# Kernel optimization log

Hardware: AMD Instinct MI355X
Metric: run time of the kernel (lower is better)

## Reference

```python
import jax, jax.numpy as jnp
import numpy as np

B, S, D, H = 2, 2048, 1024, 16
HD = D // H
LAMBDA_INIT = 0.8
EPS = 1e-5


def setup_inputs() -> dict:
    key = jax.random.key(0)
    ks = jax.random.split(key, 14)
    f32 = jnp.float32
    return {
        "inputs": jax.random.normal(ks[0], (B, S, D), f32),
        "attention_mask": jnp.ones((B, S), f32),
        "Wq": jax.random.normal(ks[1], (D, 2 * D), f32) * 0.02,
        "Wk": jax.random.normal(ks[2], (D, 2 * D), f32) * 0.02,
        "Wv": jax.random.normal(ks[3], (D, D), f32) * 0.02,
        "Wo": jax.random.normal(ks[4], (D, D), f32) * 0.02,
        "lam_q1": jax.random.normal(ks[5], (HD,), f32) * 0.1,
        "lam_q2": jax.random.normal(ks[6], (HD,), f32) * 0.1,
        "lam_k1": jax.random.normal(ks[7], (HD,), f32) * 0.1,
        "lam_k2": jax.random.normal(ks[8], (HD,), f32) * 0.1,
        "gn_weight": jnp.ones((D,), f32),
        "gn_bias": jnp.zeros((D,), f32),
        "memory_gate": jax.random.normal(ks[9], (1, H, 1, HD), f32),
        "mem": jnp.zeros((1, H, HD, HD), f32),
        "z": jnp.ones((1, H, HD, 1), f32),
    }


def reference(inputs, attention_mask, Wq, Wk, Wv, Wo, lam_q1, lam_q2, lam_k1, lam_k2,
              gn_weight, gn_bias, memory_gate, mem, z):
    Bv, Sv, Dv = inputs.shape
    scale = 1.0 / jnp.sqrt(jnp.float32(HD))
    q = (inputs @ Wq).reshape(Bv, Sv, H, 2 * HD).transpose(0, 2, 1, 3)  # B,H,S,2hd
    k = (inputs @ Wk).reshape(Bv, Sv, H, 2 * HD).transpose(0, 2, 1, 3)
    v = (inputs @ Wv).reshape(Bv, Sv, H, HD).transpose(0, 2, 1, 3)      # B,H,S,hd
    Q1, Q2 = q[..., :HD], q[..., HD:]
    K1, K2 = k[..., :HD], k[..., HD:]
    pos = jnp.arange(Sv, dtype=jnp.float32)
    slopes = 2.0 ** (-8.0 * jnp.arange(1, H + 1, dtype=jnp.float32) / H)
    alibi = slopes[None, :, None, None] * (pos[:, None] - pos[None, :])[None, None]  # 1,H,S,S
    causal = jnp.triu(jnp.full((Sv, Sv), -1e9, jnp.float32), k=1)
    pad = (1.0 - attention_mask)[:, None, None, :] * -1e9  # B,1,1,S
    def attn(Q, K):
        s = jnp.einsum('bhqd,bhkd->bhqk', Q, K) * scale - alibi + causal + pad
        return jax.nn.softmax(s, axis=-1)
    w1 = attn(Q1, K1)
    w2 = attn(Q2, K2)
    lam = jnp.exp(jnp.dot(lam_q1, lam_k1)) - jnp.exp(jnp.dot(lam_q2, lam_k2)) + LAMBDA_INIT
    diff_w = w1 - lam * w2  # B,H,S,S
    # linear-attention memory read (mem update is dead code w.r.t. output)
    sigma_q = jax.nn.elu(Q1) + 1.0
    mem_values = (sigma_q @ mem) / (sigma_q @ z)  # B,H,S,hd
    gate = jax.nn.sigmoid(memory_gate)
    out = gate * mem_values + (1.0 - gate) * jnp.einsum('bhqk,bhkd->bhqd', diff_w, v)
    # GroupNorm(num_groups=H) over channels-first layout: per (head) group stats over (hd, S)
    x = out.transpose(0, 1, 3, 2)  # B,H,hd,S
    mu = x.mean(axis=(2, 3), keepdims=True)
    var = ((x - mu) ** 2).mean(axis=(2, 3), keepdims=True)
    xn = (x - mu) / jnp.sqrt(var + EPS)
    xn = xn * gn_weight.reshape(1, H, HD, 1) + gn_bias.reshape(1, H, HD, 1)
    y = xn.transpose(0, 3, 1, 2).reshape(Bv, Sv, H * HD) * (1.0 - LAMBDA_INIT)
    return y @ Wo
```

## Files before the change

kernel.cpp:

```cpp
#include <hip/hip_runtime.h>
#include <stdint.h>

#define B_ 2
#define S_ 2048
#define D_ 1024
#define H_ 16
#define HD_ 64
#define NC_ 5120

typedef unsigned short ushort_t;
typedef __bf16 bf16x8_t __attribute__((ext_vector_type(8)));
typedef unsigned short us8 __attribute__((ext_vector_type(8)));
typedef float f32x4 __attribute__((ext_vector_type(4)));

using gq_t = const unsigned int __attribute__((address_space(1)));
using lq_t = unsigned int __attribute__((address_space(3)));

__device__ __forceinline__ unsigned short f2bf(float f) {
    unsigned u = __builtin_bit_cast(unsigned, f);
    u += 0x7fffu + ((u >> 16) & 1u);
    return (unsigned short)(u >> 16);
}
__device__ __forceinline__ float bf2f(unsigned short h) {
    unsigned u = ((unsigned)h) << 16;
    return __builtin_bit_cast(float, u);
}
__device__ __forceinline__ f32x4 mfma16(us8 a, us8 b, f32x4 c) {
    return __builtin_amdgcn_mfma_f32_16x16x32_bf16(
        __builtin_bit_cast(bf16x8_t, a), __builtin_bit_cast(bf16x8_t, b), c, 0, 0, 0);
}
__device__ __forceinline__ void gload16(const void* g, void* l) {
    __builtin_amdgcn_global_load_lds((gq_t*)g, (lq_t*)l, 16, 0, 0);
}

__global__ __launch_bounds__(256) void k_convert_x(const float* __restrict__ X,
                                                   ushort_t* __restrict__ Xb) {
    int i = (blockIdx.x * 256 + threadIdx.x) * 4;
    float4 v = *reinterpret_cast<const float4*>(X + i);
    ushort4 o;
    o.x = f2bf(v.x); o.y = f2bf(v.y); o.z = f2bf(v.z); o.w = f2bf(v.w);
    *reinterpret_cast<ushort4*>(Xb + i) = o;
}

__global__ __launch_bounds__(256) void k_transpose_w(const float* __restrict__ W,
                                                     ushort_t* __restrict__ Bt,
                                                     int N, int n_base) {
    __shared__ float lds[64 * 65];
    int n0 = blockIdx.x * 64, k0 = blockIdx.y * 64;
    int t = threadIdx.x;
#pragma unroll
    for (int i = 0; i < 16; i++) {
        int idx = i * 256 + t;
        int r = idx >> 6, c = idx & 63;
        lds[c * 65 + r] = W[(size_t)(k0 + r) * N + (n0 + c)];
    }
    __syncthreads();
#pragma unroll
    for (int i = 0; i < 16; i++) {
        int idx = i * 256 + t;
        int nn = idx >> 6, k = idx & 63;
        Bt[(size_t)(n_base + n0 + nn) * 1024 + (k0 + k)] = f2bf(lds[nn * 65 + k]);
    }
}

__device__ __forceinline__ void gemm_tile(const ushort_t* __restrict__ A,
                                          const ushort_t* __restrict__ Bt,
                                          int m0, int n0,
                                          ushort_t* ldsA, ushort_t* ldsB,
                                          f32x4 acc[4][4]) {
    const int K = 1024;
    int t = threadIdx.x;
    int w = t >> 6, l = t & 63;
    int wr = (w >> 1) * 64, wc = (w & 1) * 64;
    int lo16 = l & 15, lg = l >> 4;
#pragma unroll
    for (int m = 0; m < 4; m++)
#pragma unroll
        for (int n = 0; n < 4; n++) acc[m][n] = f32x4{0.f, 0.f, 0.f, 0.f};

    for (int k0 = 0; k0 < K; k0 += 64) {
#pragma unroll
        for (int i = 0; i < 4; i++) {
            int c = i * 256 + t;
            int row = c >> 3, co = (c & 7) * 8;
            gload16(A + (size_t)(m0 + row) * K + k0 + co, ldsA + (size_t)c * 8);
            gload16(Bt + (size_t)(n0 + row) * K + k0 + co, ldsB + (size_t)c * 8);
        }
        __syncthreads();
#pragma unroll
        for (int kk = 0; kk < 2; kk++) {
            us8 af[4], bfr[4];
#pragma unroll
            for (int m = 0; m < 4; m++)
                af[m] = *(const us8*)(ldsA + (wr + m * 16 + lo16) * 64 + kk * 32 + lg * 8);
#pragma unroll
            for (int n = 0; n < 4; n++)
                bfr[n] = *(const us8*)(ldsB + (wc + n * 16 + lo16) * 64 + kk * 32 + lg * 8);
#pragma unroll
            for (int m = 0; m < 4; m++)
#pragma unroll
                for (int n = 0; n < 4; n++)
                    acc[m][n] = mfma16(af[m], bfr[n], acc[m][n]);
        }
        __syncthreads();
    }
}

__global__ __launch_bounds__(256) void k_gemm_qkv(const ushort_t* __restrict__ Xb,
                                                  const ushort_t* __restrict__ Wt,
                                                  ushort_t* __restrict__ C) {
    __shared__ __align__(16) ushort_t ldsA[128 * 64];
    __shared__ __align__(16) ushort_t ldsB[128 * 64];
    f32x4 acc[4][4];
    int m0 = blockIdx.y * 128, n0 = blockIdx.x * 128;
    gemm_tile(Xb, Wt, m0, n0, ldsA, ldsB, acc);
    int t = threadIdx.x, w = t >> 6, l = t & 63;
    int wr = (w >> 1) * 64, wc = (w & 1) * 64, lo16 = l & 15, lg = l >> 4;
#pragma unroll
    for (int m = 0; m < 4; m++)
#pragma unroll
        for (int n = 0; n < 4; n++)
#pragma unroll
            for (int r = 0; r < 4; r++)
                C[(size_t)(m0 + wr + m * 16 + lg * 4 + r) * NC_ + (n0 + wc + n * 16 + lo16)] =
                    f2bf(acc[m][n][r]);
}

__global__ __launch_bounds__(256) void k_gemm_out(const ushort_t* __restrict__ Yb,
                                                  const ushort_t* __restrict__ Wot,
                                                  float* __restrict__ Out) {
    __shared__ __align__(16) ushort_t ldsA[128 * 64];
    __shared__ __align__(16) ushort_t ldsB[128 * 64];
    f32x4 acc[4][4];
    int m0 = blockIdx.y * 128, n0 = blockIdx.x * 128;
    gemm_tile(Yb, Wot, m0, n0, ldsA, ldsB, acc);
    int t = threadIdx.x, w = t >> 6, l = t & 63;
    int wr = (w >> 1) * 64, wc = (w & 1) * 64, lo16 = l & 15, lg = l >> 4;
#pragma unroll
    for (int m = 0; m < 4; m++)
#pragma unroll
        for (int n = 0; n < 4; n++)
#pragma unroll
            for (int r = 0; r < 4; r++)
                Out[(size_t)(m0 + wr + m * 16 + lg * 4 + r) * 1024 + (n0 + wc + n * 16 + lo16)] =
                    acc[m][n][r];
}

__global__ __launch_bounds__(256) void k_transpose_v(const ushort_t* __restrict__ C,
                                                     ushort_t* __restrict__ Vt) {
    __shared__ ushort_t lds[64 * 72];
    int bh = blockIdx.x, s0 = blockIdx.y * 64;
    int b = bh >> 4, h = bh & 15;
    const ushort_t* src = C + (size_t)(b * S_ + s0) * NC_ + 4096 + h * 64;
    ushort_t* dst = Vt + (size_t)bh * HD_ * S_ + s0;
    int t = threadIdx.x;
#pragma unroll
    for (int i = 0; i < 16; i++) {
        int idx = i * 256 + t;
        int s = idx >> 6, d = idx & 63;
        lds[d * 72 + s] = src[(size_t)s * NC_ + d];
    }
    __syncthreads();
#pragma unroll
    for (int i = 0; i < 16; i++) {
        int idx = i * 256 + t;
        int d = idx >> 6, s = idx & 63;
        dst[(size_t)d * S_ + s] = lds[d * 72 + s];
    }
}

__global__ __launch_bounds__(256, 2) void k_attn(
    const ushort_t* __restrict__ Cg, const ushort_t* __restrict__ Vtg,
    const float* __restrict__ mask,
    const float* __restrict__ lam_q1, const float* __restrict__ lam_q2,
    const float* __restrict__ lam_k1, const float* __restrict__ lam_k2,
    const float* __restrict__ mgate, const float* __restrict__ memp,
    const float* __restrict__ zp, float* __restrict__ Oatt, float* __restrict__ stats) {
    __shared__ __align__(16) ushort_t smem[2 * 12288 + 4608];
    __shared__ float ldsMaskAdj[2][64];
    ushort_t* ldsP = smem + 24576;
    ushort_t* ldsM = smem;

    int bx = blockIdx.x;
    int xcd = bx & 7, slot = bx >> 3;
    int sub = slot & 3;
    int qt = 31 - (slot >> 2);
    int h = (sub & 1) ? (15 - xcd) : xcd;
    int b = sub >> 1;
    int bh = b * 16 + h;
    int q0 = qt * 64;
    int t = threadIdx.x, w = t >> 6, l = t & 63;
    int lo16 = l & 15, lg = l >> 4;

    const ushort_t* Cb  = Cg + (size_t)(b * S_) * NC_;
    const ushort_t* Qp  = Cb + h * 128;
    const ushort_t* Kp  = Cb + 2048 + h * 128;
    const ushort_t* Vt  = Vtg + (size_t)bh * HD_ * S_;

    int qrowA = q0 + w * 16 + lo16;
    us8 q1f[2], q2f[2];
    q1f[0] = *(const us8*)(Qp + (size_t)qrowA * NC_ + lg * 8);
    q1f[1] = *(const us8*)(Qp + (size_t)qrowA * NC_ + 32 + lg * 8);
    q2f[0] = *(const us8*)(Qp + (size_t)qrowA * NC_ + 64 + lg * 8);
    q2f[1] = *(const us8*)(Qp + (size_t)qrowA * NC_ + 96 + lg * 8);

    float la = 0.f, lb = 0.f;
    for (int i = 0; i < HD_; i++) { la += lam_q1[i] * lam_k1[i]; lb += lam_q2[i] * lam_k2[i]; }
    float lam = __expf(la) - __expf(lb) + 0.8f;

    const float LOG2E = 1.4426950408889634f;
    float slope2 = exp2f(-0.5f * (float)(h + 1)) * LOG2E;
    const float scale2 = 0.125f * LOG2E;

    int qrow = q0 + w * 16 + lg * 4;
    float rowterm[4];
#pragma unroll
    for (int r = 0; r < 4; r++) rowterm[r] = -slope2 * (float)(qrow + r) - 8.0f;

    int fs = (int)floorf(((float)q0 - 63.0f - 60.0f / slope2) * (1.0f / 64.0f));
    if (fs < 0) fs = 0;

    int sx0 = (lg ^ (lo16 & 7)) * 8;
    int sx1 = ((4 + lg) ^ (lo16 & 7)) * 8;

    f32x4 o1[5], o2[5];
#pragma unroll
    for (int n = 0; n < 5; n++) { o1[n] = f32x4{0, 0, 0, 0}; o2[n] = f32x4{0, 0, 0, 0}; }

    const us8 ones8 = {0x3F80, 0x3F80, 0x3F80, 0x3F80, 0x3F80, 0x3F80, 0x3F80, 0x3F80};
    ushort_t* Pw = ldsP + w * (16 * 72);

    auto stage = [&](int buf, int kv0) {
        ushort_t* base = smem + buf * 12288;
#pragma unroll
        for (int i = 0; i < 2; i++) {
            int c = i * 256 + t, row = c >> 3;
            int co = ((c & 7) ^ (row & 7)) * 8;
            const ushort_t* krow = Kp + (size_t)(kv0 + row) * NC_;
            gload16(krow + co, base + c * 8);
            gload16(krow + 64 + co, base + 4096 + c * 8);
            gload16(Vt + (size_t)row * S_ + kv0 + co, base + 8192 + c * 8);
        }
        if (t < 64) ldsMaskAdj[buf][t] = (1.f - mask[(size_t)b * S_ + kv0 + t]) * -1.4426950e9f;
    };

    auto stream_step = [&](const ushort_t* ldsK, const ushort_t* ldsV, const us8* qf,
                           f32x4 (&oo)[5], bool diag, int kv0, const float (&colterm)[4]) {
        f32x4 s[4];
#pragma unroll
        for (int n = 0; n < 4; n++) s[n] = f32x4{0, 0, 0, 0};
        __builtin_amdgcn_s_setprio(1);
#pragma unroll
        for (int kk = 0; kk < 2; kk++) {
            int sxk = kk ? sx1 : sx0;
#pragma unroll
            for (int n = 0; n < 4; n++) {
                us8 kf = *(const us8*)(ldsK + (n * 16 + lo16) * 64 + sxk);
                s[n] = mfma16(qf[kk], kf, s[n]);
            }
        }
        __builtin_amdgcn_s_setprio(0);
#pragma unroll
        for (int n = 0; n < 4; n++)
#pragma unroll
            for (int r = 0; r < 4; r++)
                s[n][r] = fmaf(s[n][r], scale2, colterm[n] + rowterm[r]);
        if (diag) {
#pragma unroll
            for (int n = 0; n < 4; n++) {
                int kv = kv0 + n * 16 + lo16;
#pragma unroll
                for (int r = 0; r < 4; r++)
                    if (kv > qrow + r) s[n][r] = -1e30f;
            }
        }
#pragma unroll
        for (int n = 0; n < 4; n++)
#pragma unroll
            for (int r = 0; r < 4; r++)
                Pw[(lg * 4 + r) * 72 + n * 16 + lo16] = f2bf(__builtin_amdgcn_exp2f(s[n][r]));
        __builtin_amdgcn_s_setprio(1);
#pragma unroll
        for (int kk = 0; kk < 2; kk++) {
            us8 pf = *(const us8*)(Pw + lo16 * 72 + kk * 32 + lg * 8);
            oo[4] = mfma16(pf, ones8, oo[4]);
            int sxk = kk ? sx1 : sx0;
#pragma unroll
            for (int n = 0; n < 4; n++) {
                us8 vf = *(const us8*)(ldsV + (n * 16 + lo16) * 64 + sxk);
                oo[n] = mfma16(pf, vf, oo[n]);
            }
        }
        __builtin_amdgcn_s_setprio(0);
    };

    int cur = 0;
    stage(0, qt * 64);
    __syncthreads();
    for (int step = qt; step >= fs; --step) {
        if (step - 1 >= fs) stage(cur ^ 1, (step - 1) * 64);
        int kv0 = step * 64;
        float colterm[4];
#pragma unroll
        for (int n = 0; n < 4; n++)
            colterm[n] = ldsMaskAdj[cur][n * 16 + lo16] + slope2 * (float)(kv0 + n * 16 + lo16);
        bool diag = (step == qt);
        ushort_t* base = smem + cur * 12288;
        stream_step(base, base + 8192, q1f, o1, diag, kv0, colterm);
        stream_step(base + 4096, base + 8192, q2f, o2, diag, kv0, colterm);
        __syncthreads();
        cur ^= 1;
    }

    for (int i = t; i < 80 * 64; i += 256) {
        int n = i >> 6, kd = i & 63;
        float v = 0.f;
        if (n < 64) v = memp[((size_t)h * 64 + kd) * 64 + n];
        else if (n == 64) v = zp[h * 64 + kd];
        ldsM[i] = f2bf(v);
    }
    __syncthreads();

    us8 sf[2];
#pragma unroll
    for (int kk = 0; kk < 2; kk++) {
#pragma unroll
        for (int j = 0; j < 8; j++) {
            float x = bf2f(q1f[kk][j]);
            float e = (x > 0.f) ? x : (__expf(x) - 1.f);
            sf[kk][j] = f2bf(e + 1.f);
        }
    }
    f32x4 mv[5];
#pragma unroll
    for (int n = 0; n < 5; n++) mv[n] = f32x4{0, 0, 0, 0};
#pragma unroll
    for (int kk = 0; kk < 2; kk++)
#pragma unroll
        for (int n = 0; n < 5; n++) {
            us8 mb = *(const us8*)(ldsM + (n * 16 + lo16) * 64 + kk * 32 + lg * 8);
            mv[n] = mfma16(sf[kk], mb, mv[n]);
        }
    float denom[4];
#pragma unroll
    for (int r = 0; r < 4; r++) denom[r] = __shfl(mv[4][r], lg * 16);

    float gsum = 0.f, gsq = 0.f;
#pragma unroll
    for (int n = 0; n < 4; n++) {
        int d = n * 16 + lo16;
        float gate = 1.f / (1.f + __expf(-mgate[h * HD_ + d]));
#pragma unroll
        for (int r = 0; r < 4; r++) {
            int q = q0 + w * 16 + lg * 4 + r;
            float dmv = mv[n][r] / denom[r];
            float oa = o1[n][r] / o1[4][r] - lam * (o2[n][r] / o2[4][r]);
            float val = gate * dmv + (1.f - gate) * oa;
            Oatt[((size_t)bh * S_ + q) * HD_ + d] = val;
            gsum += val;
            gsq += val * val;
        }
    }
#pragma unroll
    for (int off = 1; off < 64; off <<= 1) {
        gsum += __shfl_xor(gsum, off);
        gsq += __shfl_xor(gsq, off);
    }
    if (l == 0) {
        atomicAdd(&stats[bh * 2 + 0], gsum);
        atomicAdd(&stats[bh * 2 + 1], gsq);
    }
}

__global__ __launch_bounds__(256) void k_norm(const float* __restrict__ Oatt,
                                              const float* __restrict__ stats,
                                              const float* __restrict__ gw,
                                              const float* __restrict__ gb,
                                              ushort_t* __restrict__ Yb) {
    int i4 = (blockIdx.x * 256 + threadIdx.x) * 4;
    int bh = i4 >> 17;
    int rest = i4 & 131071;
    int s = rest >> 6, d = rest & 63;
    int b = bh >> 4, h = bh & 15;
    float mu = stats[bh * 2] * (1.f / 131072.f);
    float var = stats[bh * 2 + 1] * (1.f / 131072.f) - mu * mu;
    float rstd = rsqrtf(var + 1e-5f);
    float4 v = *reinterpret_cast<const float4*>(Oatt + i4);
    int c = h * 64 + d;
    ushort4 o;
    o.x = f2bf(((v.x - mu) * rstd * gw[c + 0] + gb[c + 0]) * 0.2f);
    o.y = f2bf(((v.y - mu) * rstd * gw[c + 1] + gb[c + 1]) * 0.2f);
    o.z = f2bf(((v.z - mu) * rstd * gw[c + 2] + gb[c + 2]) * 0.2f);
    o.w = f2bf(((v.w - mu) * rstd * gw[c + 3] + gb[c + 3]) * 0.2f);
    *reinterpret_cast<ushort4*>(Yb + ((size_t)(b * S_ + s)) * 1024 + c) = o;
}

extern "C" void kernel_launch(void* const* d_in, const int* in_sizes, int n_in,
                              void* d_out, int out_size, void* d_ws, size_t ws_size,
                              hipStream_t stream) {
    const float* X      = (const float*)d_in[0];
    const float* mask   = (const float*)d_in[1];
    const float* Wq     = (const float*)d_in[2];
    const float* Wk     = (const float*)d_in[3];
    const float* Wv     = (const float*)d_in[4];
    const float* Wo     = (const float*)d_in[5];
    const float* lam_q1 = (const float*)d_in[6];
    const float* lam_q2 = (const float*)d_in[7];
    const float* lam_k1 = (const float*)d_in[8];
    const float* lam_k2 = (const float*)d_in[9];
    const float* gw     = (const float*)d_in[10];
    const float* gb     = (const float*)d_in[11];
    const float* mgate  = (const float*)d_in[12];
    const float* memp   = (const float*)d_in[13];
    const float* zp     = (const float*)d_in[14];

    char* p = (char*)d_ws;
    auto alloc = [&](size_t bytes) -> char* {
        char* r = p;
        p += (bytes + 255) & ~(size_t)255;
        return r;
    };
    ushort_t* Xb  = (ushort_t*)alloc((size_t)4096 * 1024 * 2);
    ushort_t* Wt  = (ushort_t*)alloc((size_t)5120 * 1024 * 2);
    ushort_t* Wot = (ushort_t*)alloc((size_t)1024 * 1024 * 2);
    ushort_t* C   = (ushort_t*)alloc((size_t)4096 * NC_ * 2);
    ushort_t* Vt  = (ushort_t*)alloc((size_t)B_ * H_ * S_ * HD_ * 2);
    float*    Oat = (float*)alloc((size_t)B_ * H_ * S_ * HD_ * 4);
    ushort_t* Yb  = (ushort_t*)alloc((size_t)4096 * 1024 * 2);
    float*    st  = (float*)alloc(256);

    k_convert_x<<<4096, 256, 0, stream>>>(X, Xb);
    k_transpose_w<<<dim3(32, 16), 256, 0, stream>>>(Wq, Wt, 2048, 0);
    k_transpose_w<<<dim3(32, 16), 256, 0, stream>>>(Wk, Wt, 2048, 2048);
    k_transpose_w<<<dim3(16, 16), 256, 0, stream>>>(Wv, Wt, 1024, 4096);
    k_transpose_w<<<dim3(16, 16), 256, 0, stream>>>(Wo, Wot, 1024, 0);
    k_gemm_qkv<<<dim3(40, 32), 256, 0, stream>>>(Xb, Wt, C);
    k_transpose_v<<<dim3(32, 32), 256, 0, stream>>>(C, Vt);
    hipMemsetAsync(st, 0, 64 * sizeof(float), stream);
    k_attn<<<1024, 256, 0, stream>>>(C, Vt, mask, lam_q1, lam_q2,
                                     lam_k1, lam_k2, mgate, memp, zp, Oat, st);
    k_norm<<<4096, 256, 0, stream>>>(Oat, st, gw, gb, Yb);
    k_gemm_out<<<dim3(8, 32), 256, 0, stream>>>(Yb, Wot, (float*)d_out);
}
```

Measured before the change: 216.9 us.

## Keep attention probabilities in registers via transposed QK^T and permuted K rows

Computes S^T (K as the A operand) so each lane holds the scores for one query. K rows are loaded in a permuted order so the MFMA output fragment can be packed directly with v_cvt_pk_bf16 into the A-operand layout of the PV MFMA. This removes the per-wave LDS round trip for P and frees that LDS. The column bias (ALiBi plus mask) is precomputed per permuted key into LDS, and launch bounds are raised to 3 blocks per SM. The two heads' PV MFMAs are interleaved to share V fragment loads, at the cost of more live registers.

```diff
diff --git a/kernel.cpp b/kernel.cpp
--- a/kernel.cpp
+++ b/kernel.cpp
@@ -12,6 +12,7 @@
 typedef __bf16 bf16x8_t __attribute__((ext_vector_type(8)));
 typedef unsigned short us8 __attribute__((ext_vector_type(8)));
 typedef float f32x4 __attribute__((ext_vector_type(4)));
+typedef unsigned int u32x4 __attribute__((ext_vector_type(4)));
 
 using gq_t = const unsigned int __attribute__((address_space(1)));
 using lq_t = unsigned int __attribute__((address_space(3)));
@@ -25,12 +26,20 @@
     unsigned u = ((unsigned)h) << 16;
     return __builtin_bit_cast(float, u);
 }
+__device__ __forceinline__ unsigned cvt_pk_bf16(float lo, float hi) {
+    unsigned r;
+    asm("v_cvt_pk_bf16_f32 %0, %1, %2" : "=v"(r) : "v"(lo), "v"(hi));
+    return r;
+}
 __device__ __forceinline__ f32x4 mfma16(us8 a, us8 b, f32x4 c) {
     return __builtin_amdgcn_mfma_f32_16x16x32_bf16(
         __builtin_bit_cast(bf16x8_t, a), __builtin_bit_cast(bf16x8_t, b), c, 0, 0, 0);
 }
 __device__ __forceinline__ void gload16(const void* g, void* l) {
     __builtin_amdgcn_global_load_lds((gq_t*)g, (lq_t*)l, 16, 0, 0);
+}
+__device__ __forceinline__ int invpi(int p) {
+    return (p & 0x20) | ((p & 0x0C) << 1) | ((p & 0x10) >> 2) | (p & 3);
 }
 
 __global__ __launch_bounds__(256) void k_convert_x(const float* __restrict__ X,
@@ -169,16 +178,15 @@
     }
 }
 
-__global__ __launch_bounds__(256, 2) void k_attn(
+__global__ __launch_bounds__(256, 3) void k_attn(
     const ushort_t* __restrict__ Cg, const ushort_t* __restrict__ Vtg,
     const float* __restrict__ mask,
     const float* __restrict__ lam_q1, const float* __restrict__ lam_q2,
     const float* __restrict__ lam_k1, const float* __restrict__ lam_k2,
     const float* __restrict__ mgate, const float* __restrict__ memp,
     const float* __restrict__ zp, float* __restrict__ Oatt, float* __restrict__ stats) {
-    __shared__ __align__(16) ushort_t smem[2 * 12288 + 4608];
-    __shared__ float ldsMaskAdj[2][64];
-    ushort_t* ldsP = smem + 24576;
+    __shared__ __align__(16) ushort_t smem[2 * 12288];
+    __shared__ __align__(16) float ldsAdj[2][64];
     ushort_t* ldsM = smem;
 
     int bx = blockIdx.x;
@@ -212,10 +220,12 @@
     float slope2 = exp2f(-0.5f * (float)(h + 1)) * LOG2E;
     const float scale2 = 0.125f * LOG2E;
 
-    int qrow = q0 + w * 16 + lg * 4;
-    float rowterm[4];
-#pragma unroll
-    for (int r = 0; r < 4; r++) rowterm[r] = -slope2 * (float)(qrow + r) - 8.0f;
+    int qcol = q0 + w * 16 + lo16;
+    float qterm = -slope2 * (float)qcol - 8.0f;
+
+    int koff[4];
+#pragma unroll
+    for (int n = 0; n < 4; n++) koff[n] = ((n >> 1) << 5) | (lg << 3) | ((n & 1) << 2);
 
     int fs = (int)floorf(((float)q0 - 63.0f - 60.0f / slope2) * (1.0f / 64.0f));
     if (fs < 0) fs = 0;
@@ -228,7 +238,6 @@
     for (int n = 0; n < 5; n++) { o1[n] = f32x4{0, 0, 0, 0}; o2[n] = f32x4{0, 0, 0, 0}; }
 
     const us8 ones8 = {0x3F80, 0x3F80, 0x3F80, 0x3F80, 0x3F80, 0x3F80, 0x3F80, 0x3F80};
-    ushort_t* Pw = ldsP + w * (16 * 72);
 
     auto stage = [&](int buf, int kv0) {
         ushort_t* base = smem + buf * 12288;
@@ -236,16 +245,21 @@
         for (int i = 0; i < 2; i++) {
             int c = i * 256 + t, row = c >> 3;
             int co = ((c & 7) ^ (row & 7)) * 8;
-            const ushort_t* krow = Kp + (size_t)(kv0 + row) * NC_;
+            int kvsrc = kv0 + invpi(row);
+            const ushort_t* krow = Kp + (size_t)kvsrc * NC_;
             gload16(krow + co, base + c * 8);
             gload16(krow + 64 + co, base + 4096 + c * 8);
             gload16(Vt + (size_t)row * S_ + kv0 + co, base + 8192 + c * 8);
         }
-        if (t < 64) ldsMaskAdj[buf][t] = (1.f - mask[(size_t)b * S_ + kv0 + t]) * -1.4426950e9f;
+        if (t < 64) {
+            int kvloc = invpi(t);
+            ldsAdj[buf][t] = (1.f - mask[(size_t)b * S_ + kv0 + kvloc]) * -1.4426950e9f +
+                             slope2 * (float)(kv0 + kvloc);
+        }
     };
 
-    auto stream_step = [&](const ushort_t* ldsK, const ushort_t* ldsV, const us8* qf,
-                           f32x4 (&oo)[5], bool diag, int kv0, const float (&colterm)[4]) {
+    auto score_pack = [&](const ushort_t* ldsK, const us8* qf, bool diag, int kv0,
+                          const f32x4 (&madj)[4], us8 (&pa)[2]) {
         f32x4 s[4];
 #pragma unroll
         for (int n = 0; n < 4; n++) s[n] = f32x4{0, 0, 0, 0};
@@ -256,7 +270,7 @@
 #pragma unroll
             for (int n = 0; n < 4; n++) {
                 us8 kf = *(const us8*)(ldsK + (n * 16 + lo16) * 64 + sxk);
-                s[n] = mfma16(qf[kk], kf, s[n]);
+                s[n] = mfma16(kf, qf[kk], s[n]);
             }
         }
         __builtin_amdgcn_s_setprio(0);
@@ -264,34 +278,30 @@
         for (int n = 0; n < 4; n++)
 #pragma unroll
             for (int r = 0; r < 4; r++)
-                s[n][r] = fmaf(s[n][r], scale2, colterm[n] + rowterm[r]);
+                s[n][r] = fmaf(s[n][r], scale2, madj[n][r] + qterm);
         if (diag) {
 #pragma unroll
             for (int n = 0; n < 4; n++) {
-                int kv = kv0 + n * 16 + lo16;
+                int kvn = kv0 + koff[n];
 #pragma unroll
                 for (int r = 0; r < 4; r++)
-                    if (kv > qrow + r) s[n][r] = -1e30f;
+                    if (kvn + r > qcol) s[n][r] = -1e30f;
             }
         }
+        float p[4][4];
 #pragma unroll
         for (int n = 0; n < 4; n++)
 #pragma unroll
-            for (int r = 0; r < 4; r++)
-                Pw[(lg * 4 + r) * 72 + n * 16 + lo16] = f2bf(__builtin_amdgcn_exp2f(s[n][r]));
-        __builtin_amdgcn_s_setprio(1);
+            for (int r = 0; r < 4; r++) p[n][r] = __builtin_amdgcn_exp2f(s[n][r]);
 #pragma unroll
         for (int kk = 0; kk < 2; kk++) {
-            us8 pf = *(const us8*)(Pw + lo16 * 72 + kk * 32 + lg * 8);
-            oo[4] = mfma16(pf, ones8, oo[4]);
-            int sxk = kk ? sx1 : sx0;
-#pragma unroll
-            for (int n = 0; n < 4; n++) {
-                us8 vf = *(const us8*)(ldsV + (n * 16 + lo16) * 64 + sxk);
-                oo[n] = mfma16(pf, vf, oo[n]);
-            }
-        }
-        __builtin_amdgcn_s_setprio(0);
+            u32x4 u;
+            u[0] = cvt_pk_bf16(p[2 * kk][0], p[2 * kk][1]);
+            u[1] = cvt_pk_bf16(p[2 * kk][2], p[2 * kk][3]);
+            u[2] = cvt_pk_bf16(p[2 * kk + 1][0], p[2 * kk + 1][1]);
+            u[3] = cvt_pk_bf16(p[2 * kk + 1][2], p[2 * kk + 1][3]);
+            pa[kk] = __builtin_bit_cast(us8, u);
+        }
     };
 
     int cur = 0;
@@ -300,14 +310,33 @@
     for (int step = qt; step >= fs; --step) {
         if (step - 1 >= fs) stage(cur ^ 1, (step - 1) * 64);
         int kv0 = step * 64;
-        float colterm[4];
+        ushort_t* base = smem + cur * 12288;
+        const ushort_t* ldsV = base + 8192;
+
+        f32x4 madj[4];
 #pragma unroll
         for (int n = 0; n < 4; n++)
-            colterm[n] = ldsMaskAdj[cur][n * 16 + lo16] + slope2 * (float)(kv0 + n * 16 + lo16);
+            madj[n] = *(const f32x4*)(&ldsAdj[cur][n * 16 + lg * 4]);
+
         bool diag = (step == qt);
-        ushort_t* base = smem + cur * 12288;
-        stream_step(base, base + 8192, q1f, o1, diag, kv0, colterm);
-        stream_step(base + 4096, base + 8192, q2f, o2, diag, kv0, colterm);
+        us8 pa1[2], pa2[2];
+        score_pack(base, q1f, diag, kv0, madj, pa1);
+        score_pack(base + 4096, q2f, diag, kv0, madj, pa2);
+
+        __builtin_amdgcn_s_setprio(1);
+#pragma unroll
+        for (int kk = 0; kk < 2; kk++) {
+            o1[4] = mfma16(pa1[kk], ones8, o1[4]);
+            o2[4] = mfma16(pa2[kk], ones8, o2[4]);
+            int sxk = kk ? sx1 : sx0;
+#pragma unroll
+            for (int n = 0; n < 4; n++) {
+                us8 vf = *(const us8*)(ldsV + (n * 16 + lo16) * 64 + sxk);
+                o1[n] = mfma16(pa1[kk], vf, o1[n]);
+                o2[n] = mfma16(pa2[kk], vf, o2[n]);
+            }
+        }
+        __builtin_amdgcn_s_setprio(0);
         __syncthreads();
         cur ^= 1;
     }
```

Measured after the change: 204.6 us. 1.06x faster.
